# Optimization experiments

Measured on AMD Instinct MI355X. Metric: run time of the kernel, lower is better.

## Reference

```python
import jax, jax.numpy as jnp
import numpy as np

N_AGENTS = 8
N_ACTIONS = 16
SAMPLE = 16
STATE_DIM = 256
EMBED = 256
IN_DIM = N_AGENTS * N_ACTIONS + STATE_DIM  # 384


def setup_inputs() -> dict:
    key = jax.random.key(0)
    ks = jax.random.split(key, 12)
    bs, t = 32, 32
    s = 0.05
    return {
        "states": jax.random.normal(ks[0], (bs, t, STATE_DIM), jnp.float32),
        "agent_qs": jax.random.normal(ks[1], (bs, t, N_AGENTS, N_ACTIONS), jnp.float32),
        "W1": jax.random.normal(ks[2], (IN_DIM, EMBED), jnp.float32) * s,
        "b1": jnp.zeros((EMBED,), jnp.float32),
        "W2": jax.random.normal(ks[3], (EMBED, EMBED), jnp.float32) * s,
        "b2": jnp.zeros((EMBED,), jnp.float32),
        "W3": jax.random.normal(ks[4], (EMBED, 1), jnp.float32) * s,
        "b3": jnp.zeros((1,), jnp.float32),
        "Vw1": jax.random.normal(ks[5], (STATE_DIM, EMBED), jnp.float32) * s,
        "Vb1": jnp.zeros((EMBED,), jnp.float32),
        "Vw2": jax.random.normal(ks[6], (EMBED, 1), jnp.float32) * s,
        "Vb2": jnp.zeros((1,), jnp.float32),
    }


def reference(states, agent_qs, W1, b1, W2, b2, W3, b3, Vw1, Vb1, Vw2, Vb2):
    bs, t = states.shape[0], states.shape[1]
    B = bs * t
    A, NA, S, sd = N_AGENTS, N_ACTIONS, SAMPLE, STATE_DIM
    st = states.reshape(B, sd)
    qs = agent_qs.reshape(B, A, NA)

    # --- sample grand coalitions (random permutation per (B,S) row) ---
    perm_key = jax.random.key(42)
    u = jax.random.uniform(perm_key, (B, S, A))
    pos = jnp.argsort(u, axis=-1)          # grand_coalitions_pos: agent i -> position pos[i]
    inv = jnp.argsort(pos, axis=-1)        # grand_coalitions: position j -> agent inv[j]

    indiv = jax.nn.one_hot(pos, A, dtype=st.dtype)                         # (B,S,A,A)
    subcoal = (jnp.arange(A)[None, None, None, :] <= pos[..., None]).astype(st.dtype)
    no_i = subcoal - indiv                                                 # coalition members excl. self

    # reorder agent qs along position dim: reordered[b,s,j,:] = qs[b, inv[b,s,j], :]
    reordered = jnp.take_along_axis(
        jnp.broadcast_to(qs[:, None], (B, S, A, NA)), inv[..., None], axis=2)

    # (B,S,A,A,NA): detach contribution of other coalition members
    coal = (jax.lax.stop_gradient(reordered[:, :, None] * no_i[..., None])
            + reordered[:, :, None] * indiv[..., None])

    x = coal.reshape(B * S * A, A * NA)
    stx = jnp.broadcast_to(st[:, None, None], (B, S, A, sd)).reshape(B * S * A, sd)
    inp = jnp.concatenate([stx, x], axis=1)

    h = jax.nn.relu(inp @ W1 + b1)
    h = jax.nn.relu(h @ W2 + b2)
    advs = h @ W3 + b3
    v = jax.nn.relu(stx @ Vw1 + Vb1) @ Vw2 + Vb2

    marginal = (advs + v).reshape(B, S, A)
    shapley = marginal.mean(axis=1)        # mean over samples
    return shapley.reshape(bs, t, A)
```

## Files before the change

kernel.cpp:

```cpp
#include <hip/hip_runtime.h>


#define A_N   8
#define NA_N  16
#define S_N   16
#define SD    256
#define EMB   256
#define B_TOT 1024

typedef __bf16 bf16x8 __attribute__((ext_vector_type(8)));
typedef float  f32x4  __attribute__((ext_vector_type(4)));

__device__ __forceinline__ f32x4 splat4(float v) {
  f32x4 x; x[0] = v; x[1] = v; x[2] = v; x[3] = v; return x;
}
__device__ __forceinline__ bf16x8 zero8() {
  bf16x8 z;
#pragma unroll
  for (int j = 0; j < 8; ++j) z[j] = (__bf16)0.0f;
  return z;
}

__device__ __forceinline__ float jax_uniform(unsigned idx) {
  const unsigned ks0 = 0u, ks1 = 42u, ks2 = 0x1BD11BDAu ^ 42u;
  unsigned x0 = 0u + ks0;
  unsigned x1 = idx + ks1;
#define TF_RND(r) { x0 += x1; x1 = (x1 << (r)) | (x1 >> (32 - (r))); x1 ^= x0; }
  TF_RND(13) TF_RND(15) TF_RND(26) TF_RND(6)  x0 += ks1; x1 += ks2 + 1u;
  TF_RND(17) TF_RND(29) TF_RND(16) TF_RND(24) x0 += ks2; x1 += ks0 + 2u;
  TF_RND(13) TF_RND(15) TF_RND(26) TF_RND(6)  x0 += ks0; x1 += ks1 + 3u;
  TF_RND(17) TF_RND(29) TF_RND(16) TF_RND(24) x0 += ks1; x1 += ks2 + 4u;
  TF_RND(13) TF_RND(15) TF_RND(26) TF_RND(6)  x0 += ks2; x1 += ks0 + 5u;
#undef TF_RND
  const unsigned bits = x0 ^ x1;
  return __uint_as_float((bits >> 9) | 0x3F800000u) - 1.0f;
}

__global__ __launch_bounds__(256) void prep_pack_kernel(
    const float* __restrict__ states, const float* __restrict__ W1,
    const float* __restrict__ b1, const float* __restrict__ Vw1,
    const float* __restrict__ Vb1, const float* __restrict__ Vw2,
    const float* __restrict__ Vb2, const float* __restrict__ W2,
    float* __restrict__ sW, float* __restrict__ vout,
    __bf16* __restrict__ W1b_bf, __bf16* __restrict__ W2_bf) {
  __shared__ float st_l[2][SD];
  __shared__ float red_l[2][4];

  if (blockIdx.x >= 512) {
    const int ts = (blockIdx.x - 512) * 256 + threadIdx.x;
    if (ts < 4096) {
      const int t = ts >> 10, rem = ts & 1023, u = rem >> 6, Lp = rem & 63;
      const int qp = Lp >> 4, l15p = Lp & 15;
#pragma unroll
      for (int j = 0; j < 8; ++j) {
        const int k = t * 32 + qp * 8 + j, nn = u * 16 + l15p;
        W1b_bf[ts * 8 + j] = (__bf16)W1[(SD + k) * EMB + nn];
      }
    } else {
      const int ts2 = ts - 4096;
      const int t = ts2 >> 10, rem = ts2 & 1023, u = rem >> 6, Lp = rem & 63;
      const int qp = Lp >> 4, l15p = Lp & 15;
#pragma unroll
      for (int j = 0; j < 8; ++j) {
        const int k = t * 32 + qp * 8 + j, nn = u * 16 + l15p;
        W2_bf[ts2 * 8 + j] = (__bf16)W2[k * EMB + nn];
      }
    }
    return;
  }

  const int b0 = blockIdx.x * 2;
  const int n = threadIdx.x;

#pragma unroll
  for (int i = 0; i < 2; ++i) st_l[i][n] = states[(b0 + i) * SD + n];
  __syncthreads();

  float aS[2], aV[2];
  const float b1n = b1[n], vb1n = Vb1[n];
#pragma unroll
  for (int i = 0; i < 2; ++i) { aS[i] = b1n; aV[i] = vb1n; }

#pragma unroll 8
  for (int k = 0; k < SD; ++k) {
    const float wv = W1[k * EMB + n];
    const float vw = Vw1[k * EMB + n];
#pragma unroll
    for (int i = 0; i < 2; ++i) {
      const float s = st_l[i][k];
      aS[i] = fmaf(s, wv, aS[i]);
      aV[i] = fmaf(s, vw, aV[i]);
    }
  }
#pragma unroll
  for (int i = 0; i < 2; ++i) sW[(b0 + i) * EMB + n] = aS[i];

  const float vw2 = Vw2[n];
#pragma unroll
  for (int i = 0; i < 2; ++i) {
    float c = fmaxf(aV[i], 0.f) * vw2;
#pragma unroll
    for (int off = 32; off; off >>= 1) c += __shfl_down(c, off);
    if ((n & 63) == 0) red_l[i][n >> 6] = c;
  }
  __syncthreads();
  if (n < 2)
    vout[b0 + n] = red_l[n][0] + red_l[n][1] + red_l[n][2] + red_l[n][3] + Vb2[0];
}

__global__ __launch_bounds__(256, 4) void main_kernel(
    const float* __restrict__ agent_qs, const float* __restrict__ b2g,
    const float* __restrict__ W3, const float* __restrict__ b3,
    const float* __restrict__ sW, const float* __restrict__ vv,
    const __bf16* __restrict__ W1b_bf, const __bf16* __restrict__ W2_bf,
    float* __restrict__ out) {
  __shared__ bf16x8 h1_l[32 * 64];
  __shared__ __attribute__((aligned(16))) __bf16 qs_bf[A_N * NA_N];
  __shared__ float u_l[128];
  __shared__ int   inv_l[128];
  __shared__ int   pos_l[128];
  __shared__ float adv_part[4][64];
  __shared__ float marg_l[128];

  const int b = blockIdx.x;
  const int n = threadIdx.x;
  const int w = n >> 6, L = n & 63, q = L >> 4, l15 = L & 15;
  const int s7 = l15 & 7;
  const int sl = l15 >> 3;
  const int jq = q >> 1;
  const int na0 = (q & 1) * 8;
  const int Lsw = L ^ ((L >> 3) & 3);

  if (n < 128) {
    qs_bf[n] = (__bf16)agent_qs[b * 128 + n];
    u_l[n] = jax_uniform((unsigned)(b * 128 + n));
  }
  __syncthreads();

  if (n < 128) {
    const int s = n >> 3, a = n & 7;
    const float u = u_l[n];
    int r = 0;
#pragma unroll
    for (int a2 = 0; a2 < A_N; ++a2) {
      const float u2 = u_l[s * 8 + a2];
      r += (u2 < u || (u2 == u && a2 < a)) ? 1 : 0;
    }
    inv_l[n] = r;
    pos_l[s * 8 + r] = a;
  }
  __syncthreads();

  const bool diag_on = (jq <= sl);

#pragma unroll 1
  for (int p = 0; p < 2; ++p) {
    const int invbase = (p * 8 + s7) * 8;

#pragma unroll 1
    for (int nh = 0; nh < 2; ++nh) {
      f32x4 acc[4][2];
#pragma unroll
      for (int i = 0; i < 2; ++i) {
        const float sv = sW[b * EMB + (w * 4 + nh * 2 + i) * 16 + l15];
#pragma unroll
        for (int mt = 0; mt < 4; ++mt) acc[mt][i] = splat4(sv);
      }
#pragma unroll
      for (int t = 0; t < 4; ++t) {
        const int ag = inv_l[invbase + 2 * t + jq];
        const bf16x8 afb = *(const bf16x8*)&qs_bf[ag * NA_N + na0];
        const bf16x8 afd = diag_on ? afb : zero8();
        bf16x8 bfr[2];
#pragma unroll
        for (int i = 0; i < 2; ++i)
          bfr[i] = *(const bf16x8*)
              &W1b_bf[((t * 16 + w * 4 + nh * 2 + i) * 64 + L) * 8];
#pragma unroll
        for (int mt = 0; mt < 4; ++mt) {
          if (mt < t) continue;
#pragma unroll
          for (int i = 0; i < 2; ++i)
            acc[mt][i] = __builtin_amdgcn_mfma_f32_16x16x32_bf16(
                (mt == t) ? afd : afb, bfr[i], acc[mt][i], 0, 0, 0);
        }
      }
      __bf16* h1e = (__bf16*)h1_l;
#pragma unroll
      for (int i = 0; i < 2; ++i) {
        const int X = w * 4 + nh * 2 + i;
        const int hi = (X & 1) * 2 + sl;
        const int xr = (q >> 1) | ((hi & 1) << 1);
#pragma unroll
        for (int mt = 0; mt < 4; ++mt) {
          const int ub = ((X >> 1) * 4 + mt) * 64 + (hi << 4);
#pragma unroll
          for (int r = 0; r < 4; ++r) {
            const float v = fmaxf(acc[mt][i][r], 0.f);
            const int u = ub + ((q * 4 + r) ^ xr);
            h1e[u * 8 + s7] = (__bf16)v;
          }
        }
      }
    }
    __syncthreads();

    float psum[4][4];
#pragma unroll
    for (int mt = 0; mt < 4; ++mt)
#pragma unroll
      for (int r = 0; r < 4; ++r) psum[mt][r] = 0.f;

#pragma unroll 1
    for (int nh = 0; nh < 2; ++nh) {
      f32x4 acc[4][2];
#pragma unroll
      for (int i = 0; i < 2; ++i) {
        const float bv = b2g[(w * 4 + nh * 2 + i) * 16 + l15];
#pragma unroll
        for (int mt = 0; mt < 4; ++mt) acc[mt][i] = splat4(bv);
      }
#pragma unroll 2
      for (int t = 0; t < 8; ++t) {
        bf16x8 bfr[2];
#pragma unroll
        for (int i = 0; i < 2; ++i)
          bfr[i] = *(const bf16x8*)
              &W2_bf[((t * 16 + w * 4 + nh * 2 + i) * 64 + L) * 8];
#pragma unroll
        for (int mt = 0; mt < 4; ++mt) {
          const bf16x8 af = h1_l[(t * 4 + mt) * 64 + Lsw];
#pragma unroll
          for (int i = 0; i < 2; ++i)
            acc[mt][i] = __builtin_amdgcn_mfma_f32_16x16x32_bf16(
                af, bfr[i], acc[mt][i], 0, 0, 0);
        }
      }
#pragma unroll
      for (int i = 0; i < 2; ++i) {
        const float w3v = W3[(w * 4 + nh * 2 + i) * 16 + l15];
#pragma unroll
        for (int mt = 0; mt < 4; ++mt)
#pragma unroll
          for (int r = 0; r < 4; ++r)
            psum[mt][r] = fmaf(fmaxf(acc[mt][i][r], 0.f), w3v, psum[mt][r]);
      }
    }

#pragma unroll
    for (int mt = 0; mt < 4; ++mt) {
#pragma unroll
      for (int r = 0; r < 4; ++r) {
        float sum = psum[mt][r];
#pragma unroll
        for (int off = 1; off < 16; off <<= 1) sum += __shfl_xor(sum, off);
        if (l15 == 0) adv_part[w][mt * 16 + q * 4 + r] = sum;
      }
    }
    __syncthreads();
    if (n < 64)
      marg_l[p * 64 + n] = adv_part[0][n] + adv_part[1][n] +
                           adv_part[2][n] + adv_part[3][n];
    __syncthreads();
  }

  if (n < A_N) {
    float sh = 0.f;
#pragma unroll
    for (int s = 0; s < S_N; ++s) {
      const int pr = pos_l[s * 8 + n];
      sh += marg_l[((s >> 3) << 6) + pr * 8 + (s & 7)];
    }
    out[b * A_N + n] = sh * (1.f / 16.f) + b3[0] + vv[b];
  }
}

extern "C" void kernel_launch(void* const* d_in, const int* in_sizes, int n_in,
                              void* d_out, int out_size, void* d_ws,
                              size_t ws_size, hipStream_t stream) {
  const float* states   = (const float*)d_in[0];
  const float* agent_qs = (const float*)d_in[1];
  const float* W1       = (const float*)d_in[2];
  const float* b1       = (const float*)d_in[3];
  const float* W2       = (const float*)d_in[4];
  const float* b2       = (const float*)d_in[5];
  const float* W3       = (const float*)d_in[6];
  const float* b3       = (const float*)d_in[7];
  const float* Vw1      = (const float*)d_in[8];
  const float* Vb1      = (const float*)d_in[9];
  const float* Vw2      = (const float*)d_in[10];
  const float* Vb2      = (const float*)d_in[11];
  float* out = (float*)d_out;

  char* ws = (char*)d_ws;
  float*  sW     = (float*)(ws);
  float*  vv     = (float*)(ws + 1048576);
  __bf16* W1b_bf = (__bf16*)(ws + 1052672);
  __bf16* W2_bf  = (__bf16*)(ws + 1118208);

  prep_pack_kernel<<<560, 256, 0, stream>>>(states, W1, b1, Vw1, Vb1, Vw2,
                                            Vb2, W2, sW, vv, W1b_bf, W2_bf);
  main_kernel<<<B_TOT, 256, 0, stream>>>(agent_qs, b2, W3, b3, sW, vv,
                                         W1b_bf, W2_bf, out);
}
```

Before: 117.2 us.

## Retile state projection to 16 rows by 32 columns per block and split V reduction

The prep kernel's state projection previously had each block handle 2 batch rows across all 256 columns. Each block now covers 16 rows by 32 columns, with each thread accumulating 2 rows. This cuts redundant global reads of W1/Vw1 by reusing each weight across 16 rows via shared memory. The value-head reduction now writes 8 per-column-group partial sums, which main_kernel sums along with Vb2 at the end. This adds a small extra read in main_kernel, and the 257-padded shared tile avoids bank conflicts.

```diff
diff --git a/kernel.cpp b/kernel.cpp
--- a/kernel.cpp
+++ b/kernel.cpp
@@ -40,11 +40,10 @@
     const float* __restrict__ states, const float* __restrict__ W1,
     const float* __restrict__ b1, const float* __restrict__ Vw1,
     const float* __restrict__ Vb1, const float* __restrict__ Vw2,
-    const float* __restrict__ Vb2, const float* __restrict__ W2,
-    float* __restrict__ sW, float* __restrict__ vout,
+    const float* __restrict__ W2,
+    float* __restrict__ sW, float* __restrict__ vpart,
     __bf16* __restrict__ W1b_bf, __bf16* __restrict__ W2_bf) {
-  __shared__ float st_l[2][SD];
-  __shared__ float red_l[2][4];
+  __shared__ float st_l[16][257];
 
   if (blockIdx.x >= 512) {
     const int ts = (blockIdx.x - 512) * 256 + threadIdx.x;
@@ -69,49 +68,53 @@
     return;
   }
 
-  const int b0 = blockIdx.x * 2;
-  const int n = threadIdx.x;
-
-#pragma unroll
-  for (int i = 0; i < 2; ++i) st_l[i][n] = states[(b0 + i) * SD + n];
+  const int bg = blockIdx.x >> 3, cg = blockIdx.x & 7;
+  const int b0 = bg * 16;
+  const int col = cg * 32 + (threadIdx.x & 31);
+  const int rl = threadIdx.x >> 5;
+
+#pragma unroll
+  for (int j = 0; j < 16; ++j) {
+    const int idx = threadIdx.x + j * 256;
+    st_l[idx >> 8][idx & 255] = states[(b0 + (idx >> 8)) * SD + (idx & 255)];
+  }
   __syncthreads();
 
-  float aS[2], aV[2];
-  const float b1n = b1[n], vb1n = Vb1[n];
-#pragma unroll
-  for (int i = 0; i < 2; ++i) { aS[i] = b1n; aV[i] = vb1n; }
-
+  float aS0 = b1[col], aS1 = aS0;
+  float aV0 = Vb1[col], aV1 = aV0;
+  const int r0 = rl, r1 = rl + 8;
 #pragma unroll 8
   for (int k = 0; k < SD; ++k) {
-    const float wv = W1[k * EMB + n];
-    const float vw = Vw1[k * EMB + n];
-#pragma unroll
-    for (int i = 0; i < 2; ++i) {
-      const float s = st_l[i][k];
-      aS[i] = fmaf(s, wv, aS[i]);
-      aV[i] = fmaf(s, vw, aV[i]);
-    }
-  }
-#pragma unroll
-  for (int i = 0; i < 2; ++i) sW[(b0 + i) * EMB + n] = aS[i];
-
-  const float vw2 = Vw2[n];
-#pragma unroll
-  for (int i = 0; i < 2; ++i) {
-    float c = fmaxf(aV[i], 0.f) * vw2;
-#pragma unroll
-    for (int off = 32; off; off >>= 1) c += __shfl_down(c, off);
-    if ((n & 63) == 0) red_l[i][n >> 6] = c;
-  }
-  __syncthreads();
-  if (n < 2)
-    vout[b0 + n] = red_l[n][0] + red_l[n][1] + red_l[n][2] + red_l[n][3] + Vb2[0];
+    const float wv = W1[k * EMB + col];
+    const float vw = Vw1[k * EMB + col];
+    const float sA = st_l[r0][k], sB = st_l[r1][k];
+    aS0 = fmaf(sA, wv, aS0);
+    aS1 = fmaf(sB, wv, aS1);
+    aV0 = fmaf(sA, vw, aV0);
+    aV1 = fmaf(sB, vw, aV1);
+  }
+  sW[(b0 + r0) * EMB + col] = aS0;
+  sW[(b0 + r1) * EMB + col] = aS1;
+
+  const float vw2 = Vw2[col];
+  float c0 = fmaxf(aV0, 0.f) * vw2;
+  float c1 = fmaxf(aV1, 0.f) * vw2;
+#pragma unroll
+  for (int off = 16; off; off >>= 1) {
+    c0 += __shfl_xor(c0, off);
+    c1 += __shfl_xor(c1, off);
+  }
+  if ((threadIdx.x & 31) == 0) {
+    vpart[(b0 + r0) * 8 + cg] = c0;
+    vpart[(b0 + r1) * 8 + cg] = c1;
+  }
 }
 
 __global__ __launch_bounds__(256, 4) void main_kernel(
     const float* __restrict__ agent_qs, const float* __restrict__ b2g,
     const float* __restrict__ W3, const float* __restrict__ b3,
-    const float* __restrict__ sW, const float* __restrict__ vv,
+    const float* __restrict__ sW, const float* __restrict__ vpart,
+    const float* __restrict__ Vb2,
     const __bf16* __restrict__ W1b_bf, const __bf16* __restrict__ W2_bf,
     float* __restrict__ out) {
   __shared__ bf16x8 h1_l[32 * 64];
@@ -271,7 +274,10 @@
       const int pr = pos_l[s * 8 + n];
       sh += marg_l[((s >> 3) << 6) + pr * 8 + (s & 7)];
     }
-    out[b * A_N + n] = sh * (1.f / 16.f) + b3[0] + vv[b];
+    float vvb = Vb2[0];
+#pragma unroll
+    for (int g = 0; g < 8; ++g) vvb += vpart[b * 8 + g];
+    out[b * A_N + n] = sh * (1.f / 16.f) + b3[0] + vvb;
   }
 }
 
@@ -294,12 +300,12 @@
 
   char* ws = (char*)d_ws;
   float*  sW     = (float*)(ws);
-  float*  vv     = (float*)(ws + 1048576);
-  __bf16* W1b_bf = (__bf16*)(ws + 1052672);
-  __bf16* W2_bf  = (__bf16*)(ws + 1118208);
+  float*  vpart  = (float*)(ws + 1048576);
+  __bf16* W1b_bf = (__bf16*)(ws + 1081344);
+  __bf16* W2_bf  = (__bf16*)(ws + 1146880);
 
   prep_pack_kernel<<<560, 256, 0, stream>>>(states, W1, b1, Vw1, Vb1, Vw2,
-                                            Vb2, W2, sW, vv, W1b_bf, W2_bf);
-  main_kernel<<<B_TOT, 256, 0, stream>>>(agent_qs, b2, W3, b3, sW, vv,
-                                         W1b_bf, W2_bf, out);
-}
+                                            W2, sW, vpart, W1b_bf, W2_bf);
+  main_kernel<<<B_TOT, 256, 0, stream>>>(agent_qs, b2, W3, b3, sW, vpart,
+                                         Vb2, W1b_bf, W2_bf, out);
+}
```

New measurement: 124.0 us. +5.8%, slower.
